# Kernel optimization log

Hardware: AMD Instinct MI355X
Metric: run time of the kernel (lower is better)

## Reference

```python
import jax, jax.numpy as jnp
import numpy as np

H = 128
P, L, C = 1024, 1024, 128
NT, NH, NA, NB, NPA, NPE = 64, 32, 64, 64, 32, 32


def _ln(x, g, b):
    m = jnp.mean(x, -1, keepdims=True)
    v = jnp.var(x, -1, keepdims=True)
    return (x - m) * jax.lax.rsqrt(v + 1e-5) * g + b


def _lrl(x, W, b, g, be):
    # Linear -> ReLU -> LayerNorm (the Sequential block used everywhere)
    return _ln(jax.nn.relu(x @ W.T + b), g, be)


def _combine(middle, margin, rel):
    # margin-middle-margin combine: aggregate related margin geos on both sides
    # rel: (M, G) 0/1 float; middle (M,h); margin (G,h)
    agg = rel @ margin                      # (M, h)
    comb = agg + middle + agg
    mask = (jnp.sum(rel, -1) >= 2.0).astype(middle.dtype)  # need two margins
    return comb, mask


def _score(sym, geo, mask, W1, b1, g, be, W2, b2):
    # pairwise sym x geo -> Linear/ReLU/LN -> Linear(h,1), masked, sigmoid
    pair = sym[:, None, :] + geo[None, :, :]          # (N, R, h)
    hdn = _lrl(pair, W1, b1, g, be)
    logits = hdn @ W2 + b2                            # (N, R)
    return jax.nn.sigmoid(jnp.where(mask[None, :] > 0, logits, -1e9))


def setup_inputs() -> dict:
    key = jax.random.key(0)
    ks = jax.random.split(key, 16)
    s = 0.02
    inp = {
        'points': jax.random.normal(ks[0], (P, H), jnp.float32),
        'lines': jax.random.normal(ks[1], (L, H), jnp.float32),
        'circles': jax.random.normal(ks[2], (C, H), jnp.float32),
        'text_symbols': jax.random.normal(ks[3], (NT, H), jnp.float32),
        'head_symbols': jax.random.normal(ks[4], (NH, H), jnp.float32),
        'angle_symbols': jax.random.normal(ks[5], (NA, H), jnp.float32),
        'bar_symbols': jax.random.normal(ks[6], (NB, H), jnp.float32),
        'parallel_symbols': jax.random.normal(ks[7], (NPA, H), jnp.float32),
        'perpendicular_symbols': jax.random.normal(ks[8], (NPE, H), jnp.float32),
        'rel_W': jax.random.normal(ks[9], (3, H, H), jnp.float32) * s,
        'rel_b': jnp.zeros((3, H), jnp.float32),
        'rel_g': jnp.ones((3, H), jnp.float32),
        'rel_be': jnp.zeros((3, H), jnp.float32),
        'gm_W': jax.random.normal(ks[10], (2, H, H), jnp.float32) * s,
        'gm_b': jnp.zeros((2, H), jnp.float32),
        'gm_g': jnp.ones((2, H), jnp.float32),
        'gm_be': jnp.zeros((2, H), jnp.float32),
        'sc_W1': jax.random.normal(ks[11], (6, H, H), jnp.float32) * s,
        'sc_b1': jnp.zeros((6, H), jnp.float32),
        'sc_g': jnp.ones((6, H), jnp.float32),
        'sc_be': jnp.zeros((6, H), jnp.float32),
        'sc_W2': jax.random.normal(ks[12], (6, H), jnp.float32) * s,
        'sc_b2': jnp.zeros((6,), jnp.float32),
        'pl_rels': jax.random.randint(ks[13], (P, L), 0, 2, jnp.int32),
        'pc_rels': jax.random.randint(ks[14], (P, C), 0, 2, jnp.int32),
    }
    return inp


def reference(points, lines, circles, text_symbols, head_symbols,
              angle_symbols, bar_symbols, parallel_symbols, perpendicular_symbols,
              rel_W, rel_b, rel_g, rel_be, gm_W, gm_b, gm_g, gm_be,
              sc_W1, sc_b1, sc_g, sc_be, sc_W2, sc_b2, pl_rels, pc_rels):
    pl = pl_rels.astype(points.dtype)            # (P, L)
    pc = pc_rels.astype(points.dtype)            # (P, C)

    # LPL: middle=points, margin=lines, rel=pl_rels
    lpl_c, lpl_m = _combine(points, lines, pl)
    LPL = _lrl(lpl_c, rel_W[0], rel_b[0], rel_g[0], rel_be[0])   # (P, h)
    # PLP: middle=lines, margin=points, rel=pl_rels.T
    plp_c, plp_m = _combine(lines, points, pl.T)
    PLP = _lrl(plp_c, rel_W[1], rel_b[1], rel_g[1], rel_be[1])   # (L, h)
    # PCP: middle=circles, margin=points, rel=pc_rels.T
    pcp_c, pcp_m = _combine(circles, points, pc.T)
    PCP = _lrl(pcp_c, rel_W[2], rel_b[2], rel_g[2], rel_be[2])   # (C, h)

    ones = lambda n: jnp.ones((n,), points.dtype)

    def gm(x):
        x = _lrl(x, gm_W[0], gm_b[0], gm_g[0], gm_be[0])
        return _lrl(x, gm_W[1], gm_b[1], gm_g[1], gm_be[1])

    # text symbols vs (P, L, LPL, PLP, PCP, head)
    geo_t = jnp.concatenate([points, lines, LPL, PLP, PCP, head_symbols], 0)
    mask_t = jnp.concatenate([ones(P), ones(L), lpl_m, plp_m, pcp_m, ones(NH)], 0)
    text = _score(text_symbols, gm(geo_t), mask_t,
                  sc_W1[0], sc_b1[0], sc_g[0], sc_be[0], sc_W2[0], sc_b2[0])

    # head symbols vs (P, LPL, PLP, PCP)
    geo_h = jnp.concatenate([points, LPL, PLP, PCP], 0)
    mask_h = jnp.concatenate([ones(P), lpl_m, plp_m, pcp_m], 0)
    head = _score(head_symbols, gm(geo_h), mask_h,
                  sc_W1[1], sc_b1[1], sc_g[1], sc_be[1], sc_W2[1], sc_b2[1])

    angle = _score(angle_symbols, LPL, lpl_m,
                   sc_W1[2], sc_b1[2], sc_g[2], sc_be[2], sc_W2[2], sc_b2[2])
    bar = _score(bar_symbols, PLP, plp_m,
                 sc_W1[3], sc_b1[3], sc_g[3], sc_be[3], sc_W2[3], sc_b2[3])
    para = _score(parallel_symbols, lines, ones(L),
                  sc_W1[4], sc_b1[4], sc_g[4], sc_be[4], sc_W2[4], sc_b2[4])
    perp = _score(perpendicular_symbols, LPL, lpl_m,
                  sc_W1[5], sc_b1[5], sc_g[5], sc_be[5], sc_W2[5], sc_b2[5])

    return jnp.concatenate([text.ravel(), head.ravel(), angle.ravel(),
                            bar.ravel(), para.ravel(), perp.ravel()])
```

## Files before the change

### kernel.cpp

```cpp
#include <hip/hip_runtime.h>

#define HH 128

constexpr int OFF_AGGPL = 0;
constexpr int OFF_AGGLP = OFF_AGGPL + 1024*HH;
constexpr int OFF_AGGCP = OFF_AGGLP + 1024*HH;
constexpr int OFF_MLPL  = OFF_AGGCP + 128*HH;
constexpr int OFF_MPLP  = OFF_MLPL + 1024;
constexpr int OFF_MPCP  = OFF_MPLP + 1024;
constexpr int OFF_LPL   = OFF_MPCP + 128;
constexpr int OFF_PLP   = OFF_LPL + 1024*HH;
constexpr int OFF_PCP   = OFF_PLP + 1024*HH;
constexpr int OFF_G1    = OFF_PCP + 128*HH;
constexpr int OFF_GT    = OFF_G1 + 4256*HH;
constexpr int OFF_BTEXT = OFF_GT + 4256*HH;
constexpr int OFF_BHEAD = OFF_BTEXT + 4256*HH;
constexpr int OFF_BANG  = OFF_BHEAD + 3200*HH;
constexpr int OFF_BBAR  = OFF_BANG + 1024*HH;
constexpr int OFF_BPARA = OFF_BBAR + 1024*HH;
constexpr int OFF_BPERP = OFF_BPARA + 1024*HH;
constexpr int OFF_A     = OFF_BPERP + 1024*HH;
constexpr int WS_FLOATS = OFF_A + 288*HH;

__global__ __launch_bounds__(512) void k_agg(
    const int* __restrict__ pl, const int* __restrict__ pc,
    const float* __restrict__ points, const float* __restrict__ lines,
    float* __restrict__ ws)
{
    __shared__ __attribute__((aligned(16))) float smem[16384];
    float (*rel)[1024] = (float(*)[1024])smem;
    float* red = smem;
    const int t = threadIdx.x;
    const int b = blockIdx.x;
    const int hq  = t & 31;
    const int grp = t >> 5;

    const float* V; float* OUT; float* MASK; int base;
    if (b < 128) {
        base = b*8; V = lines; OUT = ws + OFF_AGGPL; MASK = ws + OFF_MLPL;
        const int4* pl4 = (const int4*)pl;
        #pragma unroll
        for (int i = 0; i < 4; ++i) {
            int idx = i*512 + t; int r = idx >> 8, lq = idx & 255;
            int4 v = pl4[(base + r)*256 + lq];
            float4 f; f.x=(float)v.x; f.y=(float)v.y; f.z=(float)v.z; f.w=(float)v.w;
            *(float4*)&rel[r][lq*4] = f;
        }
    } else if (b < 256) {
        base = (b-128)*8; V = points; OUT = ws + OFF_AGGLP; MASK = ws + OFF_MPLP;
        #pragma unroll
        for (int i = 0; i < 16; ++i) {
            int idx = i*512 + t; int c = idx & 7, k = idx >> 3;
            rel[c][k] = (float)pl[k*1024 + base + c];
        }
    } else {
        base = (b-256)*8; V = points; OUT = ws + OFF_AGGCP; MASK = ws + OFF_MPCP;
        #pragma unroll
        for (int i = 0; i < 16; ++i) {
            int idx = i*512 + t; int c = idx & 7, k = idx >> 3;
            rel[c][k] = (float)pc[k*128 + base + c];
        }
    }
    __syncthreads();
    {
        int r = t >> 6, lane = t & 63;
        float s = 0.f;
        #pragma unroll
        for (int i = 0; i < 16; ++i) s += rel[r][lane*16 + i];
        #pragma unroll
        for (int off = 32; off; off >>= 1) s += __shfl_xor(s, off, 64);
        if (lane == 0) MASK[base + r] = (s >= 2.0f) ? 1.0f : 0.0f;
    }

    float4 acc[8];
    #pragma unroll
    for (int r = 0; r < 8; ++r) acc[r] = {0.f, 0.f, 0.f, 0.f};
    const float4* V4 = (const float4*)V;
    const int l0 = grp * 64;
    #pragma unroll 4
    for (int l = l0; l < l0 + 64; l += 4) {
        float4 v0 = V4[(l+0)*32 + hq];
        float4 v1 = V4[(l+1)*32 + hq];
        float4 v2 = V4[(l+2)*32 + hq];
        float4 v3 = V4[(l+3)*32 + hq];
        #pragma unroll
        for (int r = 0; r < 8; ++r) {
            float4 rv = *(const float4*)&rel[r][l];
            acc[r].x += rv.x*v0.x + rv.y*v1.x + rv.z*v2.x + rv.w*v3.x;
            acc[r].y += rv.x*v0.y + rv.y*v1.y + rv.z*v2.y + rv.w*v3.y;
            acc[r].z += rv.x*v0.z + rv.y*v1.z + rv.z*v2.z + rv.w*v3.z;
            acc[r].w += rv.x*v0.w + rv.y*v1.w + rv.z*v2.w + rv.w*v3.w;
        }
    }
    __syncthreads();
    #pragma unroll
    for (int r = 0; r < 8; ++r)
        *(float4*)&red[(grp*8 + r)*128 + hq*4] = acc[r];
    __syncthreads();
    #pragma unroll
    for (int o = t; o < 1024; o += 512) {
        int r = o >> 7, c = o & 127;
        float s = 0.f;
        #pragma unroll
        for (int g2 = 0; g2 < 16; ++g2) s += red[g2*1024 + r*128 + c];
        OUT[(base + r)*HH + c] = s;
    }
}

__global__ __launch_bounds__(512) void k_lrl(
    int mode, float* __restrict__ ws,
    const float* __restrict__ points, const float* __restrict__ lines,
    const float* __restrict__ circles, const float* __restrict__ text_s,
    const float* __restrict__ head_s, const float* __restrict__ angle_s,
    const float* __restrict__ bar_s, const float* __restrict__ para_s,
    const float* __restrict__ perp_s,
    const float* __restrict__ rel_W, const float* __restrict__ rel_b,
    const float* __restrict__ rel_g, const float* __restrict__ rel_be,
    const float* __restrict__ gm_W, const float* __restrict__ gm_b,
    const float* __restrict__ gm_g, const float* __restrict__ gm_be,
    const float* __restrict__ sc_W1, const float* __restrict__ sc_b1)
{
    __shared__ __attribute__((aligned(16))) float Xs[32][132];
    __shared__ __attribute__((aligned(16))) float Ws[64][132];
    const int t = threadIdx.x;
    const int row0 = blockIdx.x * 32;

    const float* W = nullptr; const float* bias = nullptr;
    const float* gv = nullptr; const float* bev = nullptr;
    const float* xsrc = nullptr; const float* asrc = nullptr; const float* msrc = nullptr;
    float* outp = nullptr;
    bool do_ln = false;

    if (mode == 0) {
        do_ln = true;
        if (row0 < 1024) {
            asrc = ws + OFF_AGGPL + row0*HH; msrc = points + row0*HH;
            W = rel_W;          bias = rel_b;       gv = rel_g;       bev = rel_be;
            outp = ws + OFF_LPL + row0*HH;
        } else if (row0 < 2048) {
            int r = row0 - 1024;
            asrc = ws + OFF_AGGLP + r*HH; msrc = lines + r*HH;
            W = rel_W + 16384;  bias = rel_b + 128; gv = rel_g + 128; bev = rel_be + 128;
            outp = ws + OFF_PLP + r*HH;
        } else {
            int r = row0 - 2048;
            asrc = ws + OFF_AGGCP + r*HH; msrc = circles + r*HH;
            W = rel_W + 32768;  bias = rel_b + 256; gv = rel_g + 256; bev = rel_be + 256;
            outp = ws + OFF_PCP + r*HH;
        }
    } else if (mode == 1) {
        do_ln = true; W = gm_W; bias = gm_b; gv = gm_g; bev = gm_be;
        outp = ws + OFF_G1 + row0*HH;
        if      (row0 < 1024) xsrc = points + row0*HH;
        else if (row0 < 2048) xsrc = lines + (row0-1024)*HH;
        else if (row0 < 3072) xsrc = ws + OFF_LPL + (row0-2048)*HH;
        else if (row0 < 4096) xsrc = ws + OFF_PLP + (row0-3072)*HH;
        else if (row0 < 4224) xsrc = ws + OFF_PCP + (row0-4096)*HH;
        else                  xsrc = head_s + (row0-4224)*HH;
    } else if (mode == 2) {
        do_ln = true; W = gm_W + 16384; bias = gm_b + 128; gv = gm_g + 128; bev = gm_be + 128;
        xsrc = ws + OFF_G1 + row0*HH;
        outp = ws + OFF_GT + row0*HH;
    } else {
        do_ln = false;
        if (row0 < 4256) {
            xsrc = ws + OFF_GT + row0*HH; W = sc_W1; outp = ws + OFF_BTEXT + row0*HH;
        } else if (row0 < 7456) {
            int i0 = row0 - 4256;
            W = sc_W1 + 16384; outp = ws + OFF_BHEAD + i0*HH;
            int gtrow;
            if      (i0 < 1024) gtrow = i0;
            else if (i0 < 2048) gtrow = 2048 + (i0 - 1024);
            else if (i0 < 3072) gtrow = 3072 + (i0 - 2048);
            else                gtrow = 4096 + (i0 - 3072);
            xsrc = ws + OFF_GT + gtrow*HH;
        } else if (row0 < 8480) {
            int i0 = row0 - 7456;
            xsrc = ws + OFF_LPL + i0*HH; W = sc_W1 + 2*16384; outp = ws + OFF_BANG + i0*HH;
        } else if (row0 < 9504) {
            int i0 = row0 - 8480;
            xsrc = ws + OFF_PLP + i0*HH; W = sc_W1 + 3*16384; outp = ws + OFF_BBAR + i0*HH;
        } else if (row0 < 10528) {
            int i0 = row0 - 9504;
            xsrc = lines + i0*HH;        W = sc_W1 + 4*16384; outp = ws + OFF_BPARA + i0*HH;
        } else if (row0 < 11552) {
            int i0 = row0 - 10528;
            xsrc = ws + OFF_LPL + i0*HH; W = sc_W1 + 5*16384; outp = ws + OFF_BPERP + i0*HH;
        } else {
            int i0 = row0 - 11552;
            outp = ws + OFF_A + i0*HH;
            int k; const float* s;
            if      (i0 < 64)  { k=0; s = text_s  + i0*HH; }
            else if (i0 < 96)  { k=1; s = head_s  + (i0-64)*HH; }
            else if (i0 < 160) { k=2; s = angle_s + (i0-96)*HH; }
            else if (i0 < 224) { k=3; s = bar_s   + (i0-160)*HH; }
            else if (i0 < 256) { k=4; s = para_s  + (i0-224)*HH; }
            else               { k=5; s = perp_s  + (i0-256)*HH; }
            xsrc = s; W = sc_W1 + k*16384; bias = sc_b1 + k*128;
        }
    }

    if (asrc != nullptr) {
        #pragma unroll
        for (int i = 0; i < 2; ++i) {
            int idx = i*512 + t; int r = idx >> 5, hq = idx & 31;
            float4 a = *(const float4*)&asrc[r*HH + hq*4];
            float4 m = *(const float4*)&msrc[r*HH + hq*4];
            float4 v; v.x = 2.f*a.x+m.x; v.y = 2.f*a.y+m.y; v.z = 2.f*a.z+m.z; v.w = 2.f*a.w+m.w;
            *(float4*)&Xs[r][hq*4] = v;
        }
    } else {
        #pragma unroll
        for (int i = 0; i < 2; ++i) {
            int idx = i*512 + t; int r = idx >> 5, hq = idx & 31;
            *(float4*)&Xs[r][hq*4] = *(const float4*)&xsrc[r*HH + hq*4];
        }
    }

    const int jq = t & 31;
    const int rq = t >> 5;
    float acc[2][4] = {};
    for (int p = 0; p < 2; ++p) {
        __syncthreads();
        #pragma unroll
        for (int i = 0; i < 4; ++i) {
            int idx = i*512 + t; int j = idx >> 4, hq = idx & 15;
            float4 v = *(const float4*)&W[j*HH + p*64 + hq*4];
            Ws[hq*4+0][j] = v.x; Ws[hq*4+1][j] = v.y; Ws[hq*4+2][j] = v.z; Ws[hq*4+3][j] = v.w;
        }
        __syncthreads();
        #pragma unroll
        for (int hh = 0; hh < 64; hh += 4) {
            const int h = p*64 + hh;
            float4 x0 = *(const float4*)&Xs[rq*2+0][h];
            float4 x1 = *(const float4*)&Xs[rq*2+1][h];
            float4 w0 = *(const float4*)&Ws[hh+0][jq*4];
            float4 w1 = *(const float4*)&Ws[hh+1][jq*4];
            float4 w2 = *(const float4*)&Ws[hh+2][jq*4];
            float4 w3 = *(const float4*)&Ws[hh+3][jq*4];
            #define ROWUPD(ri, xv) \
                acc[ri][0] += xv.x*w0.x + xv.y*w1.x + xv.z*w2.x + xv.w*w3.x; \
                acc[ri][1] += xv.x*w0.y + xv.y*w1.y + xv.z*w2.y + xv.w*w3.y; \
                acc[ri][2] += xv.x*w0.z + xv.y*w1.z + xv.z*w2.z + xv.w*w3.z; \
                acc[ri][3] += xv.x*w0.w + xv.y*w1.w + xv.z*w2.w + xv.w*w3.w;
            ROWUPD(0, x0) ROWUPD(1, x1)
            #undef ROWUPD
        }
    }

    float4 bv = {0.f,0.f,0.f,0.f};
    if (bias != nullptr) bv = *(const float4*)&bias[jq*4];
    if (do_ln) {
        float4 gg = *(const float4*)&gv[jq*4];
        float4 bb = *(const float4*)&bev[jq*4];
        #pragma unroll
        for (int ri = 0; ri < 2; ++ri) {
            float y0 = fmaxf(acc[ri][0] + bv.x, 0.f);
            float y1 = fmaxf(acc[ri][1] + bv.y, 0.f);
            float y2 = fmaxf(acc[ri][2] + bv.z, 0.f);
            float y3 = fmaxf(acc[ri][3] + bv.w, 0.f);
            float s1 = y0+y1+y2+y3;
            float s2 = y0*y0+y1*y1+y2*y2+y3*y3;
            #pragma unroll
            for (int off = 16; off; off >>= 1) {
                s1 += __shfl_xor(s1, off, 32);
                s2 += __shfl_xor(s2, off, 32);
            }
            float m   = s1 * (1.0f/128.0f);
            float var = s2 * (1.0f/128.0f) - m*m;
            float sc  = rsqrtf(var + 1e-5f);
            float4 o;
            o.x = (y0 - m)*sc*gg.x + bb.x;
            o.y = (y1 - m)*sc*gg.y + bb.y;
            o.z = (y2 - m)*sc*gg.z + bb.z;
            o.w = (y3 - m)*sc*gg.w + bb.w;
            *(float4*)&outp[(rq*2+ri)*HH + jq*4] = o;
        }
    } else {
        #pragma unroll
        for (int ri = 0; ri < 2; ++ri) {
            float4 o;
            o.x = acc[ri][0] + bv.x; o.y = acc[ri][1] + bv.y;
            o.z = acc[ri][2] + bv.z; o.w = acc[ri][3] + bv.w;
            *(float4*)&outp[(rq*2+ri)*HH + jq*4] = o;
        }
    }
}

__global__ __launch_bounds__(256, 4) void k_score(
    const float* __restrict__ ws,
    const float* __restrict__ sc_g, const float* __restrict__ sc_be,
    const float* __restrict__ sc_W2, const float* __restrict__ sc_b2,
    float* __restrict__ out)
{
    __shared__ __attribute__((aligned(16))) float As[32][140];
    __shared__ __attribute__((aligned(16))) float Bs[32][140];
    __shared__ __attribute__((aligned(16))) float gw2s[128];
    __shared__ float msk[32];
    __shared__ float red2[4];
    const int t = threadIdx.x, b = blockIdx.x;
    int k, tn, tr, Rk, Abase, outbase;
    const float* Bk;
    if (b < 266)      { k=0; int lc=b;     tn=lc/133; tr=lc%133; Rk=4256; Abase=0;   outbase=0;      Bk = ws+OFF_BTEXT; }
    else if (b < 366) { k=1; int lc=b-266; tn=0;      tr=lc;     Rk=3200; Abase=64;  outbase=272384; Bk = ws+OFF_BHEAD; }
    else if (b < 430) { k=2; int lc=b-366; tn=lc>>5;  tr=lc&31;  Rk=1024; Abase=96;  outbase=374784; Bk = ws+OFF_BANG; }
    else if (b < 494) { k=3; int lc=b-430; tn=lc>>5;  tr=lc&31;  Rk=1024; Abase=160; outbase=440320; Bk = ws+OFF_BBAR; }
    else if (b < 526) { k=4; int lc=b-494; tn=0;      tr=lc;     Rk=1024; Abase=224; outbase=505856; Bk = ws+OFF_BPARA; }
    else              { k=5; int lc=b-526; tn=0;      tr=lc;     Rk=1024; Abase=256; outbase=538624; Bk = ws+OFF_BPERP; }

    if (t < 128) {
        float g = sc_g[k*128+t], w2 = sc_W2[k*128+t], be = sc_be[k*128+t];
        float gw = g*w2, bw = be*w2;
        gw2s[t] = gw;
        #pragma unroll
        for (int off = 32; off; off >>= 1) {
            gw += __shfl_xor(gw, off, 64);
            bw += __shfl_xor(bw, off, 64);
        }
        if ((t & 63) == 0) { red2[(t>>6)*2+0] = gw; red2[(t>>6)*2+1] = bw; }
    }
    const float* Ap = ws + OFF_A + (Abase + tn*32)*HH;
    const float* Bp = Bk + tr*32*HH;
    #pragma unroll
    for (int i = 0; i < 4; ++i) {
        int idx = i*256 + t; int r = idx >> 5, hq = idx & 31;
        *(float4*)&As[r][hq*4] = *(const float4*)&Ap[r*HH + hq*4];
        *(float4*)&Bs[r][hq*4] = *(const float4*)&Bp[r*HH + hq*4];
    }
    if (t < 32) {
        int r = tr*32 + t;
        float mv = 1.0f;
        const float* mL = ws + OFF_MLPL;
        const float* mP = ws + OFF_MPLP;
        const float* mC = ws + OFF_MPCP;
        if (k == 0) {
            if      (r >= 2048 && r < 3072) mv = mL[r-2048];
            else if (r >= 3072 && r < 4096) mv = mP[r-3072];
            else if (r >= 4096 && r < 4224) mv = mC[r-4096];
        } else if (k == 1) {
            if      (r >= 1024 && r < 2048) mv = mL[r-1024];
            else if (r >= 2048 && r < 3072) mv = mP[r-2048];
            else if (r >= 3072)             mv = mC[r-3072];
        } else if (k == 2 || k == 5) mv = mL[r];
        else if (k == 3)             mv = mP[r];
        msk[t] = mv;
    }
    __syncthreads();
    const float sgw2 = red2[0] + red2[2];
    const float cb   = red2[1] + red2[3] + sc_b2[k];
    const int n2 = t >> 4;
    const int r2 = t & 15;
    float s1[4] = {}, s2[4] = {}, sw[4] = {};
    #pragma unroll 4
    for (int h = 0; h < 128; h += 4) {
        float4 a0 = *(const float4*)&As[n2*2+0][h];
        float4 a1 = *(const float4*)&As[n2*2+1][h];
        float4 b0 = *(const float4*)&Bs[r2*2+0][h];
        float4 b1 = *(const float4*)&Bs[r2*2+1][h];
        float4 wv = *(const float4*)&gw2s[h];
        float y;
        #define PUPD(pi, av, bv2) \
            y = fmaxf(av.x + bv2.x, 0.f); s1[pi] += y; s2[pi] += y*y; sw[pi] += y*wv.x; \
            y = fmaxf(av.y + bv2.y, 0.f); s1[pi] += y; s2[pi] += y*y; sw[pi] += y*wv.y; \
            y = fmaxf(av.z + bv2.z, 0.f); s1[pi] += y; s2[pi] += y*y; sw[pi] += y*wv.z; \
            y = fmaxf(av.w + bv2.w, 0.f); s1[pi] += y; s2[pi] += y*y; sw[pi] += y*wv.w;
        PUPD(0, a0, b0) PUPD(1, a0, b1) PUPD(2, a1, b0) PUPD(3, a1, b1)
        #undef PUPD
    }
    #pragma unroll
    for (int pi = 0; pi < 4; ++pi) {
        int ni = n2*2 + (pi >> 1);
        int ri = r2*2 + (pi & 1);
        float m   = s1[pi] * (1.0f/128.0f);
        float var = s2[pi] * (1.0f/128.0f) - m*m;
        float logit = (sw[pi] - m*sgw2) * rsqrtf(var + 1e-5f) + cb;
        float o = (msk[ri] > 0.f) ? (1.0f/(1.0f + __expf(-logit))) : 0.0f;
        out[outbase + (tn*32+ni)*Rk + tr*32 + ri] = o;
    }
}

extern "C" void kernel_launch(void* const* d_in, const int* in_sizes, int n_in,
                              void* d_out, int out_size, void* d_ws, size_t ws_size,
                              hipStream_t stream)
{
    const float* points  = (const float*)d_in[0];
    const float* lines   = (const float*)d_in[1];
    const float* circles = (const float*)d_in[2];
    const float* text_s  = (const float*)d_in[3];
    const float* head_s  = (const float*)d_in[4];
    const float* angle_s = (const float*)d_in[5];
    const float* bar_s   = (const float*)d_in[6];
    const float* para_s  = (const float*)d_in[7];
    const float* perp_s  = (const float*)d_in[8];
    const float* rel_W   = (const float*)d_in[9];
    const float* rel_b   = (const float*)d_in[10];
    const float* rel_g   = (const float*)d_in[11];
    const float* rel_be  = (const float*)d_in[12];
    const float* gm_W    = (const float*)d_in[13];
    const float* gm_b    = (const float*)d_in[14];
    const float* gm_g    = (const float*)d_in[15];
    const float* gm_be   = (const float*)d_in[16];
    const float* sc_W1   = (const float*)d_in[17];
    const float* sc_b1   = (const float*)d_in[18];
    const float* sc_g    = (const float*)d_in[19];
    const float* sc_be   = (const float*)d_in[20];
    const float* sc_W2   = (const float*)d_in[21];
    const float* sc_b2   = (const float*)d_in[22];
    const int*   pl      = (const int*)d_in[23];
    const int*   pc      = (const int*)d_in[24];
    float* ws  = (float*)d_ws;
    float* out = (float*)d_out;
    if (ws_size < (size_t)WS_FLOATS * sizeof(float)) return;

    hipLaunchKernelGGL(k_agg, dim3(272), dim3(512), 0, stream, pl, pc, points, lines, ws);
    #define LRL_ARGS ws, points, lines, circles, text_s, head_s, angle_s, bar_s, para_s, perp_s, \
        rel_W, rel_b, rel_g, rel_be, gm_W, gm_b, gm_g, gm_be, sc_W1, sc_b1
    hipLaunchKernelGGL(k_lrl, dim3(68),  dim3(512), 0, stream, 0, LRL_ARGS);
    hipLaunchKernelGGL(k_lrl, dim3(133), dim3(512), 0, stream, 1, LRL_ARGS);
    hipLaunchKernelGGL(k_lrl, dim3(133), dim3(512), 0, stream, 2, LRL_ARGS);
    hipLaunchKernelGGL(k_lrl, dim3(370), dim3(512), 0, stream, 3, LRL_ARGS);
    #undef LRL_ARGS
    hipLaunchKernelGGL(k_score, dim3(558), dim3(256), 0, stream, ws, sc_g, sc_be, sc_W2, sc_b2, out);
}
```

Measured before the change: 197.9 us.

## Fuse second geo-mapping layer with text/head score projections; merge independent lrl launches

The second gm LRL layer now runs in a new k_gt kernel that keeps the GT tile in shared memory and immediately applies the text and head sc_W1 projections, so the GT intermediate is never written to or re-read from global memory. The first gm layer and the independent angle/bar/para/perp/symbol projections are merged into a single k_lrl launch (mode 4), cutting the launch count from four to two. This removes the GT workspace buffer and launch gaps. In exchange, k_gt does up to three sequential matmuls per block on only 133 blocks, which may leave the GPU underoccupied.

```diff
diff --git a/kernel.cpp b/kernel.cpp
--- a/kernel.cpp
+++ b/kernel.cpp
@@ -12,8 +12,7 @@
 constexpr int OFF_PLP   = OFF_LPL + 1024*HH;
 constexpr int OFF_PCP   = OFF_PLP + 1024*HH;
 constexpr int OFF_G1    = OFF_PCP + 128*HH;
-constexpr int OFF_GT    = OFF_G1 + 4256*HH;
-constexpr int OFF_BTEXT = OFF_GT + 4256*HH;
+constexpr int OFF_BTEXT = OFF_G1 + 4256*HH;
 constexpr int OFF_BHEAD = OFF_BTEXT + 4256*HH;
 constexpr int OFF_BANG  = OFF_BHEAD + 3200*HH;
 constexpr int OFF_BBAR  = OFF_BANG + 1024*HH;
@@ -106,6 +105,43 @@
         OUT[(base + r)*HH + c] = s;
     }
 }
+
+#define STAGE_X_PLAIN(src) \
+    _Pragma("unroll") \
+    for (int i = 0; i < 2; ++i) { \
+        int idx = i*512 + t; int r = idx >> 5, hq2 = idx & 31; \
+        *(float4*)&Xs[r][hq2*4] = *(const float4*)&(src)[r*HH + hq2*4]; \
+    }
+
+#define MATMUL_2x4(Wp, accv) \
+    for (int p = 0; p < 2; ++p) { \
+        __syncthreads(); \
+        _Pragma("unroll") \
+        for (int i = 0; i < 4; ++i) { \
+            int idx = i*512 + t; int j = idx >> 4, hq2 = idx & 15; \
+            float4 v = *(const float4*)&(Wp)[j*HH + p*64 + hq2*4]; \
+            Ws[hq2*4+0][j] = v.x; Ws[hq2*4+1][j] = v.y; Ws[hq2*4+2][j] = v.z; Ws[hq2*4+3][j] = v.w; \
+        } \
+        __syncthreads(); \
+        _Pragma("unroll") \
+        for (int hh = 0; hh < 64; hh += 4) { \
+            const int h = p*64 + hh; \
+            float4 x0 = *(const float4*)&Xs[rq*2+0][h]; \
+            float4 x1 = *(const float4*)&Xs[rq*2+1][h]; \
+            float4 w0 = *(const float4*)&Ws[hh+0][jq*4]; \
+            float4 w1 = *(const float4*)&Ws[hh+1][jq*4]; \
+            float4 w2 = *(const float4*)&Ws[hh+2][jq*4]; \
+            float4 w3 = *(const float4*)&Ws[hh+3][jq*4]; \
+            accv[0][0] += x0.x*w0.x + x0.y*w1.x + x0.z*w2.x + x0.w*w3.x; \
+            accv[0][1] += x0.x*w0.y + x0.y*w1.y + x0.z*w2.y + x0.w*w3.y; \
+            accv[0][2] += x0.x*w0.z + x0.y*w1.z + x0.z*w2.z + x0.w*w3.z; \
+            accv[0][3] += x0.x*w0.w + x0.y*w1.w + x0.z*w2.w + x0.w*w3.w; \
+            accv[1][0] += x1.x*w0.x + x1.y*w1.x + x1.z*w2.x + x1.w*w3.x; \
+            accv[1][1] += x1.x*w0.y + x1.y*w1.y + x1.z*w2.y + x1.w*w3.y; \
+            accv[1][2] += x1.x*w0.z + x1.y*w1.z + x1.z*w2.z + x1.w*w3.z; \
+            accv[1][3] += x1.x*w0.w + x1.y*w1.w + x1.z*w2.w + x1.w*w3.w; \
+        } \
+    }
 
 __global__ __launch_bounds__(512) void k_lrl(
     int mode, float* __restrict__ ws,
@@ -123,7 +159,6 @@
     __shared__ __attribute__((aligned(16))) float Xs[32][132];
     __shared__ __attribute__((aligned(16))) float Ws[64][132];
     const int t = threadIdx.x;
-    const int row0 = blockIdx.x * 32;
 
     const float* W = nullptr; const float* bias = nullptr;
     const float* gv = nullptr; const float* bev = nullptr;
@@ -132,6 +167,7 @@
     bool do_ln = false;
 
     if (mode == 0) {
+        int row0 = blockIdx.x * 32;
         do_ln = true;
         if (row0 < 1024) {
             asrc = ws + OFF_AGGPL + row0*HH; msrc = points + row0*HH;
@@ -148,55 +184,43 @@
             W = rel_W + 32768;  bias = rel_b + 256; gv = rel_g + 256; bev = rel_be + 256;
             outp = ws + OFF_PCP + r*HH;
         }
-    } else if (mode == 1) {
-        do_ln = true; W = gm_W; bias = gm_b; gv = gm_g; bev = gm_be;
-        outp = ws + OFF_G1 + row0*HH;
-        if      (row0 < 1024) xsrc = points + row0*HH;
-        else if (row0 < 2048) xsrc = lines + (row0-1024)*HH;
-        else if (row0 < 3072) xsrc = ws + OFF_LPL + (row0-2048)*HH;
-        else if (row0 < 4096) xsrc = ws + OFF_PLP + (row0-3072)*HH;
-        else if (row0 < 4224) xsrc = ws + OFF_PCP + (row0-4096)*HH;
-        else                  xsrc = head_s + (row0-4224)*HH;
-    } else if (mode == 2) {
-        do_ln = true; W = gm_W + 16384; bias = gm_b + 128; gv = gm_g + 128; bev = gm_be + 128;
-        xsrc = ws + OFF_G1 + row0*HH;
-        outp = ws + OFF_GT + row0*HH;
     } else {
-        do_ln = false;
-        if (row0 < 4256) {
-            xsrc = ws + OFF_GT + row0*HH; W = sc_W1; outp = ws + OFF_BTEXT + row0*HH;
-        } else if (row0 < 7456) {
-            int i0 = row0 - 4256;
-            W = sc_W1 + 16384; outp = ws + OFF_BHEAD + i0*HH;
-            int gtrow;
-            if      (i0 < 1024) gtrow = i0;
-            else if (i0 < 2048) gtrow = 2048 + (i0 - 1024);
-            else if (i0 < 3072) gtrow = 3072 + (i0 - 2048);
-            else                gtrow = 4096 + (i0 - 3072);
-            xsrc = ws + OFF_GT + gtrow*HH;
-        } else if (row0 < 8480) {
-            int i0 = row0 - 7456;
-            xsrc = ws + OFF_LPL + i0*HH; W = sc_W1 + 2*16384; outp = ws + OFF_BANG + i0*HH;
-        } else if (row0 < 9504) {
-            int i0 = row0 - 8480;
-            xsrc = ws + OFF_PLP + i0*HH; W = sc_W1 + 3*16384; outp = ws + OFF_BBAR + i0*HH;
-        } else if (row0 < 10528) {
-            int i0 = row0 - 9504;
-            xsrc = lines + i0*HH;        W = sc_W1 + 4*16384; outp = ws + OFF_BPARA + i0*HH;
-        } else if (row0 < 11552) {
-            int i0 = row0 - 10528;
-            xsrc = ws + OFF_LPL + i0*HH; W = sc_W1 + 5*16384; outp = ws + OFF_BPERP + i0*HH;
+        if (blockIdx.x < 133) {
+            int row0 = blockIdx.x * 32;
+            do_ln = true; W = gm_W; bias = gm_b; gv = gm_g; bev = gm_be;
+            outp = ws + OFF_G1 + row0*HH;
+            if      (row0 < 1024) xsrc = points + row0*HH;
+            else if (row0 < 2048) xsrc = lines + (row0-1024)*HH;
+            else if (row0 < 3072) xsrc = ws + OFF_LPL + (row0-2048)*HH;
+            else if (row0 < 4096) xsrc = ws + OFF_PLP + (row0-3072)*HH;
+            else if (row0 < 4224) xsrc = ws + OFF_PCP + (row0-4096)*HH;
+            else                  xsrc = head_s + (row0-4224)*HH;
         } else {
-            int i0 = row0 - 11552;
-            outp = ws + OFF_A + i0*HH;
-            int k; const float* s;
-            if      (i0 < 64)  { k=0; s = text_s  + i0*HH; }
-            else if (i0 < 96)  { k=1; s = head_s  + (i0-64)*HH; }
-            else if (i0 < 160) { k=2; s = angle_s + (i0-96)*HH; }
-            else if (i0 < 224) { k=3; s = bar_s   + (i0-160)*HH; }
-            else if (i0 < 256) { k=4; s = para_s  + (i0-224)*HH; }
-            else               { k=5; s = perp_s  + (i0-256)*HH; }
-            xsrc = s; W = sc_W1 + k*16384; bias = sc_b1 + k*128;
+            int i0 = (blockIdx.x - 133) * 32;
+            do_ln = false;
+            if (i0 < 1024) {
+                xsrc = ws + OFF_LPL + i0*HH;        W = sc_W1 + 2*16384; outp = ws + OFF_BANG  + i0*HH;
+            } else if (i0 < 2048) {
+                int r = i0 - 1024;
+                xsrc = ws + OFF_PLP + r*HH;         W = sc_W1 + 3*16384; outp = ws + OFF_BBAR  + r*HH;
+            } else if (i0 < 3072) {
+                int r = i0 - 2048;
+                xsrc = lines + r*HH;                W = sc_W1 + 4*16384; outp = ws + OFF_BPARA + r*HH;
+            } else if (i0 < 4096) {
+                int r = i0 - 3072;
+                xsrc = ws + OFF_LPL + r*HH;         W = sc_W1 + 5*16384; outp = ws + OFF_BPERP + r*HH;
+            } else {
+                int r = i0 - 4096;
+                outp = ws + OFF_A + r*HH;
+                int k; const float* s;
+                if      (r < 64)  { k=0; s = text_s  + r*HH; }
+                else if (r < 96)  { k=1; s = head_s  + (r-64)*HH; }
+                else if (r < 160) { k=2; s = angle_s + (r-96)*HH; }
+                else if (r < 224) { k=3; s = bar_s   + (r-160)*HH; }
+                else if (r < 256) { k=4; s = para_s  + (r-224)*HH; }
+                else              { k=5; s = perp_s  + (r-256)*HH; }
+                xsrc = s; W = sc_W1 + k*16384; bias = sc_b1 + k*128;
+            }
         }
     }
 
@@ -210,43 +234,13 @@
             *(float4*)&Xs[r][hq*4] = v;
         }
     } else {
-        #pragma unroll
-        for (int i = 0; i < 2; ++i) {
-            int idx = i*512 + t; int r = idx >> 5, hq = idx & 31;
-            *(float4*)&Xs[r][hq*4] = *(const float4*)&xsrc[r*HH + hq*4];
-        }
+        STAGE_X_PLAIN(xsrc)
     }
 
     const int jq = t & 31;
     const int rq = t >> 5;
     float acc[2][4] = {};
-    for (int p = 0; p < 2; ++p) {
-        __syncthreads();
-        #pragma unroll
-        for (int i = 0; i < 4; ++i) {
-            int idx = i*512 + t; int j = idx >> 4, hq = idx & 15;
-            float4 v = *(const float4*)&W[j*HH + p*64 + hq*4];
-            Ws[hq*4+0][j] = v.x; Ws[hq*4+1][j] = v.y; Ws[hq*4+2][j] = v.z; Ws[hq*4+3][j] = v.w;
-        }
-        __syncthreads();
-        #pragma unroll
-        for (int hh = 0; hh < 64; hh += 4) {
-            const int h = p*64 + hh;
-            float4 x0 = *(const float4*)&Xs[rq*2+0][h];
-            float4 x1 = *(const float4*)&Xs[rq*2+1][h];
-            float4 w0 = *(const float4*)&Ws[hh+0][jq*4];
-            float4 w1 = *(const float4*)&Ws[hh+1][jq*4];
-            float4 w2 = *(const float4*)&Ws[hh+2][jq*4];
-            float4 w3 = *(const float4*)&Ws[hh+3][jq*4];
-            #define ROWUPD(ri, xv) \
-                acc[ri][0] += xv.x*w0.x + xv.y*w1.x + xv.z*w2.x + xv.w*w3.x; \
-                acc[ri][1] += xv.x*w0.y + xv.y*w1.y + xv.z*w2.y + xv.w*w3.y; \
-                acc[ri][2] += xv.x*w0.z + xv.y*w1.z + xv.z*w2.z + xv.w*w3.z; \
-                acc[ri][3] += xv.x*w0.w + xv.y*w1.w + xv.z*w2.w + xv.w*w3.w;
-            ROWUPD(0, x0) ROWUPD(1, x1)
-            #undef ROWUPD
-        }
-    }
+    MATMUL_2x4(W, acc)
 
     float4 bv = {0.f,0.f,0.f,0.f};
     if (bias != nullptr) bv = *(const float4*)&bias[jq*4];
@@ -282,6 +276,82 @@
             float4 o;
             o.x = acc[ri][0] + bv.x; o.y = acc[ri][1] + bv.y;
             o.z = acc[ri][2] + bv.z; o.w = acc[ri][3] + bv.w;
+            *(float4*)&outp[(rq*2+ri)*HH + jq*4] = o;
+        }
+    }
+}
+
+__global__ __launch_bounds__(512) void k_gt(
+    float* __restrict__ ws,
+    const float* __restrict__ gm_W, const float* __restrict__ gm_b,
+    const float* __restrict__ gm_g, const float* __restrict__ gm_be,
+    const float* __restrict__ sc_W1)
+{
+    __shared__ __attribute__((aligned(16))) float Xs[32][132];
+    __shared__ __attribute__((aligned(16))) float Ws[64][132];
+    const int t = threadIdx.x;
+    const int row0 = blockIdx.x * 32;
+    const int jq = t & 31;
+    const int rq = t >> 5;
+
+    const float* xsrc = ws + OFF_G1 + row0*HH;
+    STAGE_X_PLAIN(xsrc)
+    const float* W = gm_W + 16384;
+    float acc[2][4] = {};
+    MATMUL_2x4(W, acc)
+
+    float4 bv = *(const float4*)&gm_b[128 + jq*4];
+    float4 gg = *(const float4*)&gm_g[128 + jq*4];
+    float4 bb = *(const float4*)&gm_be[128 + jq*4];
+    float gt[2][4];
+    #pragma unroll
+    for (int ri = 0; ri < 2; ++ri) {
+        float y0 = fmaxf(acc[ri][0] + bv.x, 0.f);
+        float y1 = fmaxf(acc[ri][1] + bv.y, 0.f);
+        float y2 = fmaxf(acc[ri][2] + bv.z, 0.f);
+        float y3 = fmaxf(acc[ri][3] + bv.w, 0.f);
+        float s1 = y0+y1+y2+y3;
+        float s2 = y0*y0+y1*y1+y2*y2+y3*y3;
+        #pragma unroll
+        for (int off = 16; off; off >>= 1) {
+            s1 += __shfl_xor(s1, off, 32);
+            s2 += __shfl_xor(s2, off, 32);
+        }
+        float m   = s1 * (1.0f/128.0f);
+        float var = s2 * (1.0f/128.0f) - m*m;
+        float sc  = rsqrtf(var + 1e-5f);
+        gt[ri][0] = (y0 - m)*sc*gg.x + bb.x;
+        gt[ri][1] = (y1 - m)*sc*gg.y + bb.y;
+        gt[ri][2] = (y2 - m)*sc*gg.z + bb.z;
+        gt[ri][3] = (y3 - m)*sc*gg.w + bb.w;
+    }
+    __syncthreads();
+    #pragma unroll
+    for (int ri = 0; ri < 2; ++ri)
+        *(float4*)&Xs[rq*2+ri][jq*4] = *(float4*)&gt[ri][0];
+
+    float accB[2][4] = {};
+    MATMUL_2x4(sc_W1, accB)
+    {
+        float* outp = ws + OFF_BTEXT + row0*HH;
+        #pragma unroll
+        for (int ri = 0; ri < 2; ++ri) {
+            float4 o; o.x = accB[ri][0]; o.y = accB[ri][1]; o.z = accB[ri][2]; o.w = accB[ri][3];
+            *(float4*)&outp[(rq*2+ri)*HH + jq*4] = o;
+        }
+    }
+
+    int hr0 = -1;
+    if (row0 < 1024) hr0 = row0;
+    else if (row0 >= 2048 && row0 < 4224) hr0 = row0 - 1024;
+    if (hr0 >= 0) {
+        const float* W1h = sc_W1 + 16384;
+        float accC[2][4] = {};
+        MATMUL_2x4(W1h, accC)
+        float* outp = ws + OFF_BHEAD + hr0*HH;
+        #pragma unroll
+        for (int ri = 0; ri < 2; ++ri) {
+            float4 o; o.x = accC[ri][0]; o.y = accC[ri][1]; o.z = accC[ri][2]; o.w = accC[ri][3];
             *(float4*)&outp[(rq*2+ri)*HH + jq*4] = o;
         }
     }
@@ -416,9 +486,8 @@
     #define LRL_ARGS ws, points, lines, circles, text_s, head_s, angle_s, bar_s, para_s, perp_s, \
         rel_W, rel_b, rel_g, rel_be, gm_W, gm_b, gm_g, gm_be, sc_W1, sc_b1
     hipLaunchKernelGGL(k_lrl, dim3(68),  dim3(512), 0, stream, 0, LRL_ARGS);
-    hipLaunchKernelGGL(k_lrl, dim3(133), dim3(512), 0, stream, 1, LRL_ARGS);
-    hipLaunchKernelGGL(k_lrl, dim3(133), dim3(512), 0, stream, 2, LRL_ARGS);
-    hipLaunchKernelGGL(k_lrl, dim3(370), dim3(512), 0, stream, 3, LRL_ARGS);
+    hipLaunchKernelGGL(k_lrl, dim3(270), dim3(512), 0, stream, 4, LRL_ARGS);
     #undef LRL_ARGS
+    hipLaunchKernelGGL(k_gt, dim3(133), dim3(512), 0, stream, ws, gm_W, gm_b, gm_g, gm_be, sc_W1);
     hipLaunchKernelGGL(k_score, dim3(558), dim3(256), 0, stream, ws, sc_g, sc_be, sc_W2, sc_b2, out);
 }
```

After: 205.4 us. 1.04x slower.
